# Performance work log

Hardware: AMD Instinct MI355X
Metric: run time of the kernel (lower is better)

Reference implementation:

```python
import jax, jax.numpy as jnp
import numpy as np

K = 32        # neighbors kept
SCALE = 1     # dilation stride for dilated kNN


def setup_inputs() -> dict:
    key = jax.random.key(0)
    ks = jax.random.split(key, 8)
    s = 0.05  # weight init scale
    return {
        "x": jax.random.normal(ks[0], (16, 3, 4096), jnp.float32),
        "w1": jax.random.normal(ks[1], (64, 3), jnp.float32) * s,
        "b1": jnp.zeros((64,), jnp.float32),
        "w2": jax.random.normal(ks[2], (128, 64), jnp.float32) * s,
        "b2": jnp.zeros((128,), jnp.float32),
        "w3": jax.random.normal(ks[3], (1024, 128), jnp.float32) * s,
        "b3": jnp.zeros((1024,), jnp.float32),
        "fw1": jax.random.normal(ks[4], (512, 1024), jnp.float32) * s,
        "fb1": jnp.zeros((512,), jnp.float32),
        "fw2": jax.random.normal(ks[5], (256, 512), jnp.float32) * s,
        "fb2": jnp.zeros((256,), jnp.float32),
        "fw3": jax.random.normal(ks[6], (9, 256), jnp.float32) * s,
        "fb3": jnp.zeros((9,), jnp.float32),
    }


def _knn_idx(x):
    # x: (B, C, N). Returns (B, N, K) indices of K nearest neighbors (dilated by SCALE).
    inner = jnp.einsum('bcn,bcm->bnm', x, x)            # (B, N, N)
    sq = jnp.sum(x * x, axis=1)                          # (B, N)
    neg_dist = 2.0 * inner - sq[:, :, None] - sq[:, None, :]  # = -||xi-xj||^2
    _, idx = jax.lax.top_k(neg_dist, K * SCALE)          # (B, N, K*SCALE)
    return idx[:, :, ::SCALE]                            # (B, N, K)


def reference(x, w1, b1, w2, b2, w3, b3, fw1, fb1, fw2, fb2, fw3, fb3):
    B, C, N = x.shape
    idx = _knn_idx(x)                                    # (B, N, K)
    xt = jnp.swapaxes(x, 1, 2)                           # (B, N, C)
    # gather neighbors: nbrs[b,n,k,c] = xt[b, idx[b,n,k], c]
    nbrs = jax.vmap(lambda xb, ib: xb[ib])(xt, idx)      # (B, N, K, C)
    x0 = nbrs - xt[:, :, None, :]                        # edge features x_j - x_i

    # STN (T-Net): shared MLP over edges, global max pool, FC head -> 3x3 transform
    h = jax.nn.relu(jnp.einsum('bnkc,oc->bnko', x0, w1) + b1)
    h = jax.nn.relu(jnp.einsum('bnkc,oc->bnko', h, w2) + b2)
    h = jax.nn.relu(jnp.einsum('bnkc,oc->bnko', h, w3) + b3)
    g = jnp.max(h, axis=(1, 2))                          # (B, 1024)
    f = jax.nn.relu(g @ fw1.T + fb1)
    f = jax.nn.relu(f @ fw2.T + fb2)
    t = (f @ fw3.T + fb3).reshape(B, 3, 3) + jnp.eye(3, dtype=x.dtype)

    out = jnp.einsum('bnc,bcd->bnd', xt, t)              # bmm(x^T, t)
    return jnp.swapaxes(out, 1, 2)                       # (B, 3, N)
```

## Files before the change

kernel.cpp:

```cpp
#include <hip/hip_runtime.h>
#include <hip/hip_fp8.h>

typedef __bf16 bf16_t;
typedef __bf16 bf16x8 __attribute__((ext_vector_type(8)));
typedef float floatx16 __attribute__((ext_vector_type(16)));
typedef int intx8 __attribute__((ext_vector_type(8)));
typedef unsigned long long u64;

#define B_ 16
#define N_ 4096
#define K_ 32


__device__ __forceinline__ unsigned enc_f(float f) {
    unsigned u = __float_as_uint(f);
    return (u & 0x80000000u) ? ~u : (u | 0x80000000u);
}
__device__ __forceinline__ float dec_f(unsigned e) {
    return __uint_as_float((e & 0x80000000u) ? (e & 0x7fffffffu) : ~e);
}

__global__ __launch_bounds__(512, 4) void knn_kernel(
    const float* __restrict__ x, const float* __restrict__ w3,
    const float* __restrict__ w2, unsigned short* __restrict__ idxb,
    unsigned* __restrict__ g_enc, unsigned char* __restrict__ w3f8,
    bf16_t* __restrict__ w2sw)
{
    __shared__ __align__(16) float4 cand[16 * 257];
    unsigned* lists = (unsigned*)cand;
    unsigned* m1 = ((unsigned*)cand) + 8192;
    const int tid = threadIdx.x;
    const int bid = blockIdx.x;

    {
        const int g = bid * 512 + tid;
        if (g < 131072) {
            const int q = g & 15, lI = (g >> 4) & 63, mt2 = (g >> 10) & 3, cb = g >> 12;
            const int lmI = lI & 31, hiI = lI >> 5;
            const int ch = mt2 * 32 + (q & 3) + 8 * (q >> 2) + 4 * hiI;
            __hip_fp8_e4m3 t(16.0f * w3[(cb * 32 + lmI) * 128 + ch]);
            w3f8[g] = t.__x;
        } else if (g < 139264) {
            const int o = g - 131072;
            const int f = o >> 9, r = o & 511, lI = r >> 3, jj = r & 7;
            const int ks = f & 3, nb = f >> 2, lmI = lI & 31, hiI = lI >> 5;
            w2sw[o] = (bf16_t)w2[(nb * 32 + lmI) * 64 + ks * 16 + hiI * 8 + jj];
        } else if (g < 155648) {
            g_enc[g - 139264] = 0u;
        }
    }

    const int b  = bid >> 7;
    const int q  = tid >> 4;
    const int n  = (bid & 127) * 32 + q;
    const int t  = tid & 15;
    const float* xb = x + b * 3 * N_;

    for (int j = tid; j < N_; j += 512) {
        float cx = xb[j], cy = xb[N_ + j], cz = xb[2 * N_ + j];
        cand[j + (j >> 8)] = make_float4(-2.f * cx, -2.f * cy, -2.f * cz,
                                         fmaf(cx, cx, fmaf(cy, cy, cz * cz)));
    }
    __syncthreads();

    const float xi0 = xb[n], xi1 = xb[N_ + n], xi2 = xb[2 * N_ + n];
    const float xisq1 = fmaf(xi0, xi0, fmaf(xi1, xi1, xi2 * xi2)) + 1.0f;

    unsigned r[8];
    #pragma unroll
    for (int s = 0; s < 8; s++) r[s] = 0x7F7FFFFFu;

    const int j0 = t * 256;
    const int pb = t * 257;
    #pragma unroll 8
    for (int jj = 0; jj < 256; jj++) {
        const float4 c = cand[pb + jj];
        const float d = fmaf(c.z, xi2, fmaf(c.y, xi1, fmaf(c.x, xi0, c.w)));
        const unsigned key =
            (__float_as_uint(d + xisq1) & 0xFFFFF000u) | (unsigned)(j0 + jj);
        #pragma unroll
        for (int s = 7; s >= 1; s--) {
            const unsigned hv = r[s - 1] > key ? r[s - 1] : key;
            r[s] = r[s] < hv ? r[s] : hv;
        }
        r[0] = r[0] < key ? r[0] : key;
    }
    __syncthreads();

    #pragma unroll
    for (int k = 0; k < 8; k++) lists[tid * 9 + k] = r[k];
    __syncthreads();

    if (tid < 128) {
        const int q1 = tid >> 2, gi = tid & 3;
        const int base = (q1 * 16 + gi * 4) * 9;
        unsigned h0 = lists[base], h1 = lists[base + 9];
        unsigned h2 = lists[base + 18], h3 = lists[base + 27];
        int p0 = 0, p1 = 0, p2 = 0, p3 = 0;
        unsigned* outp = m1 + (q1 * 4 + gi) * 32;
        #pragma unroll 1
        for (int k = 0; k < 32; k++) {
            const unsigned m01 = h0 < h1 ? h0 : h1;
            const unsigned m23 = h2 < h3 ? h2 : h3;
            const unsigned v = m01 < m23 ? m01 : m23;
            outp[k] = v;
            if (m01 < m23) {
                if (h1 < h0) { p1++; h1 = p1 < 8 ? lists[base + 9 + p1] : 0xFFFFFFFFu; }
                else         { p0++; h0 = p0 < 8 ? lists[base + p0]     : 0xFFFFFFFFu; }
            } else {
                if (h3 < h2) { p3++; h3 = p3 < 8 ? lists[base + 27 + p3] : 0xFFFFFFFFu; }
                else         { p2++; h2 = p2 < 8 ? lists[base + 18 + p2] : 0xFFFFFFFFu; }
            }
        }
    }
    __syncthreads();

    if (tid < 32) {
        const unsigned* g0 = m1 + tid * 128;
        unsigned h0 = g0[0], h1 = g0[32], h2 = g0[64], h3 = g0[96];
        int p0 = 0, p1 = 0, p2 = 0, p3 = 0;
        const int nq = (bid & 127) * 32 + tid;
        unsigned short* op = idxb + ((size_t)(b * N_ + nq)) * K_;
        #pragma unroll 1
        for (int k = 0; k < K_; k++) {
            const unsigned m01 = h0 < h1 ? h0 : h1;
            const unsigned m23 = h2 < h3 ? h2 : h3;
            const unsigned v = m01 < m23 ? m01 : m23;
            op[k] = (unsigned short)(v & 0xFFFu);
            if (m01 < m23) {
                if (h1 < h0) { p1++; h1 = p1 < 32 ? g0[32 + p1] : 0xFFFFFFFFu; }
                else         { p0++; h0 = p0 < 32 ? g0[p0]      : 0xFFFFFFFFu; }
            } else {
                if (h3 < h2) { p3++; h3 = p3 < 32 ? g0[96 + p3] : 0xFFFFFFFFu; }
                else         { p2++; h2 = p2 < 32 ? g0[64 + p2] : 0xFFFFFFFFu; }
            }
        }
    }
}

__device__ __forceinline__ void chunk_epilogue(
    const floatx16& a0, const floatx16& a1, int cb, unsigned* gl, int lm)
{
    float c0 = fmaxf(a0[0], a1[0]);
    float c1 = fmaxf(a0[1], a1[1]);
    float c2 = fmaxf(a0[2], a1[2]);
    float c3 = fmaxf(a0[3], a1[3]);
    #pragma unroll
    for (int o = 4; o < 16; o += 4) {
        c0 = fmaxf(fmaxf(a0[o + 0], a1[o + 0]), c0);
        c1 = fmaxf(fmaxf(a0[o + 1], a1[o + 1]), c1);
        c2 = fmaxf(fmaxf(a0[o + 2], a1[o + 2]), c2);
        c3 = fmaxf(fmaxf(a0[o + 3], a1[o + 3]), c3);
    }
    const float m = fmaxf(fmaxf(c0, c1), fmaxf(c2, c3));
    atomicMax(&gl[cb * 32 + lm], enc_f(m));
}

__global__ __launch_bounds__(256, 3) void mlp_kernel(
    const float* __restrict__ x, const unsigned short* __restrict__ idxb,
    const float* __restrict__ w1, const float* __restrict__ b1,
    const float* __restrict__ b2,
    const bf16_t* __restrict__ w2sw, const unsigned char* __restrict__ w3f8,
    unsigned* __restrict__ g_enc)
{
    __shared__ unsigned gl[1024];
    __shared__ __align__(16) float4 w1l[64];
    __shared__ __align__(16) float b2s[128];

    const int tid = threadIdx.x;
    const int b   = blockIdx.x >> 9;
    const int p0  = (blockIdx.x & 511) * 8;
    const float* xb = x + b * 3 * N_;

    const int wv = tid >> 6;
    const int l  = tid & 63;
    const int lm = l & 31;
    const int hi = l >> 5;

    for (int i = tid; i < 1024; i += 256) gl[i] = 0u;
    if (tid < 64)
        w1l[tid] = make_float4(w1[tid * 3], w1[tid * 3 + 1], w1[tid * 3 + 2], b1[tid]);
    else if (tid < 192)
        b2s[tid - 64] = 256.0f * b2[tid - 64];
    __syncthreads();

    const uint4* w3v = (const uint4*)w3f8;
    intx8 bwA[2], bwB[2];
    #pragma unroll
    for (int mt2 = 0; mt2 < 4; mt2++) {
        const uint4 v = w3v[mt2 * 64 + l];
        bwA[mt2 >> 1][(mt2 & 1) * 4 + 0] = (int)v.x;
        bwA[mt2 >> 1][(mt2 & 1) * 4 + 1] = (int)v.y;
        bwA[mt2 >> 1][(mt2 & 1) * 4 + 2] = (int)v.z;
        bwA[mt2 >> 1][(mt2 & 1) * 4 + 3] = (int)v.w;
    }

    bf16x8 b1h[2][4];
    float d0[2], d1[2], d2[2];
    #pragma unroll
    for (int nt2 = 0; nt2 < 2; nt2++) {
        const int pp = p0 + wv * 2 + nt2;
        const int j  = idxb[((size_t)(b * N_ + pp)) * K_ + lm];
        d0[nt2] = xb[j]          - xb[pp];
        d1[nt2] = xb[N_ + j]     - xb[N_ + pp];
        d2[nt2] = xb[2 * N_ + j] - xb[2 * N_ + pp];
    }
    #pragma unroll
    for (int ks = 0; ks < 4; ks++)
        #pragma unroll
        for (int jj = 0; jj < 8; jj++) {
            const float4 w = w1l[ks * 16 + hi * 8 + jj];
            #pragma unroll
            for (int nt2 = 0; nt2 < 2; nt2++)
                b1h[nt2][ks][jj] = (bf16_t)fmaxf(
                    fmaf(w.z, d2[nt2], fmaf(w.y, d1[nt2], fmaf(w.x, d0[nt2], w.w))), 0.f);
        }

    intx8 a3v[2][2];
    #pragma unroll
    for (int mt2 = 0; mt2 < 4; mt2++) {
        floatx16 acc0 = (floatx16)0.f, acc1 = (floatx16)0.f;
        #pragma unroll
        for (int ks = 0; ks < 4; ks++) {
            const bf16x8 aw = *(const bf16x8*)&w2sw[((mt2 * 4 + ks) * 64 + l) * 8];
            acc0 = __builtin_amdgcn_mfma_f32_32x32x16_bf16(aw, b1h[0][ks], acc0, 0, 0, 0);
            acc1 = __builtin_amdgcn_mfma_f32_32x32x16_bf16(aw, b1h[1][ks], acc1, 0, 0, 0);
        }
        const int kq = mt2 >> 1, c0 = (mt2 & 1) * 4;
        #pragma unroll
        for (int i2 = 0; i2 < 4; i2++) {
            const float4 bb = *(const float4*)&b2s[mt2 * 32 + i2 * 8 + hi * 4];
            {
                const float v0 = fmaxf(fmaf(acc0[4 * i2 + 0], 256.f, bb.x), 0.f);
                const float v1 = fmaxf(fmaf(acc0[4 * i2 + 1], 256.f, bb.y), 0.f);
                const float v2 = fmaxf(fmaf(acc0[4 * i2 + 2], 256.f, bb.z), 0.f);
                const float v3 = fmaxf(fmaf(acc0[4 * i2 + 3], 256.f, bb.w), 0.f);
                int w = __builtin_amdgcn_cvt_pk_fp8_f32(v0, v1, 0, false);
                w = __builtin_amdgcn_cvt_pk_fp8_f32(v2, v3, w, true);
                a3v[0][kq][c0 + i2] = w;
            }
            {
                const float v0 = fmaxf(fmaf(acc1[4 * i2 + 0], 256.f, bb.x), 0.f);
                const float v1 = fmaxf(fmaf(acc1[4 * i2 + 1], 256.f, bb.y), 0.f);
                const float v2 = fmaxf(fmaf(acc1[4 * i2 + 2], 256.f, bb.z), 0.f);
                const float v3 = fmaxf(fmaf(acc1[4 * i2 + 3], 256.f, bb.w), 0.f);
                int w = __builtin_amdgcn_cvt_pk_fp8_f32(v0, v1, 0, false);
                w = __builtin_amdgcn_cvt_pk_fp8_f32(v2, v3, w, true);
                a3v[1][kq][c0 + i2] = w;
            }
        }
    }

    const floatx16 zf = (floatx16)0.f;

#define PREFETCH_W3(dst, c) do {                                              \
        _Pragma("unroll")                                                     \
        for (int mt2 = 0; mt2 < 4; mt2++) {                                   \
            const uint4 v = w3v[((c) * 4 + mt2) * 64 + l];                    \
            dst[mt2 >> 1][(mt2 & 1) * 4 + 0] = (int)v.x;                      \
            dst[mt2 >> 1][(mt2 & 1) * 4 + 1] = (int)v.y;                      \
            dst[mt2 >> 1][(mt2 & 1) * 4 + 2] = (int)v.z;                      \
            dst[mt2 >> 1][(mt2 & 1) * 4 + 3] = (int)v.w;                      \
        } } while (0)

#define COMPUTE_W3(d0_, d1_, buf) do {                                        \
        __builtin_amdgcn_s_setprio(1);                                        \
        d0_ = __builtin_amdgcn_mfma_scale_f32_32x32x64_f8f6f4(                \
            a3v[0][0], buf[0], zf, 0, 0, 0, 0x7F7F7F7F, 0, 0x7F7F7F7F);       \
        d1_ = __builtin_amdgcn_mfma_scale_f32_32x32x64_f8f6f4(                \
            a3v[1][0], buf[0], zf, 0, 0, 0, 0x7F7F7F7F, 0, 0x7F7F7F7F);       \
        d0_ = __builtin_amdgcn_mfma_scale_f32_32x32x64_f8f6f4(                \
            a3v[0][1], buf[1], d0_, 0, 0, 0, 0x7F7F7F7F, 0, 0x7F7F7F7F);      \
        d1_ = __builtin_amdgcn_mfma_scale_f32_32x32x64_f8f6f4(                \
            a3v[1][1], buf[1], d1_, 0, 0, 0, 0x7F7F7F7F, 0, 0x7F7F7F7F);      \
        __builtin_amdgcn_s_setprio(0); } while (0)

    floatx16 pA0, pA1, pB0, pB1;

    PREFETCH_W3(bwB, 1);
    COMPUTE_W3(pA0, pA1, bwA);

    #pragma unroll 1
    for (int cc = 0; cc < 15; cc++) {
        PREFETCH_W3(bwA, 2 * cc + 2);
        COMPUTE_W3(pB0, pB1, bwB);
        chunk_epilogue(pA0, pA1, 2 * cc, gl, lm);
        PREFETCH_W3(bwB, 2 * cc + 3);
        COMPUTE_W3(pA0, pA1, bwA);
        chunk_epilogue(pB0, pB1, 2 * cc + 1, gl, lm);
    }
    COMPUTE_W3(pB0, pB1, bwB);
    chunk_epilogue(pA0, pA1, 30, gl, lm);
    chunk_epilogue(pB0, pB1, 31, gl, lm);

#undef PREFETCH_W3
#undef COMPUTE_W3

    __syncthreads();
    for (int i = tid; i < 1024; i += 256)
        atomicMax(&g_enc[b * 1024 + i], gl[i]);
}

__global__ __launch_bounds__(256) void head_kernel(
    const unsigned* __restrict__ g_enc, const float* __restrict__ b3,
    const float* __restrict__ fw1, const float* __restrict__ fb1,
    const float* __restrict__ fw2, const float* __restrict__ fb2,
    const float* __restrict__ fw3, const float* __restrict__ fb3,
    float* __restrict__ tmat)
{
    __shared__ __align__(16) float g[1024];
    __shared__ __align__(16) float f1[512];
    __shared__ __align__(16) float f2[256];
    const int t = threadIdx.x, b = blockIdx.x;

    for (int i = t; i < 1024; i += 256)
        g[i] = fmaxf(fmaf(dec_f(g_enc[b * 1024 + i]), 2.44140625e-4f, b3[i]), 0.f);
    __syncthreads();

    for (int o = t; o < 512; o += 256) {
        const float4* wr = (const float4*)(fw1 + (size_t)o * 1024);
        const float4* gv = (const float4*)g;
        float acc = fb1[o];
        for (int i = 0; i < 256; i++) {
            float4 a = wr[i], c = gv[i];
            acc = fmaf(a.x, c.x, acc); acc = fmaf(a.y, c.y, acc);
            acc = fmaf(a.z, c.z, acc); acc = fmaf(a.w, c.w, acc);
        }
        f1[o] = fmaxf(acc, 0.f);
    }
    __syncthreads();
    {
        const int o = t;
        const float4* wr = (const float4*)(fw2 + (size_t)o * 512);
        const float4* fv = (const float4*)f1;
        float acc = fb2[o];
        for (int i = 0; i < 128; i++) {
            float4 a = wr[i], c = fv[i];
            acc = fmaf(a.x, c.x, acc); acc = fmaf(a.y, c.y, acc);
            acc = fmaf(a.z, c.z, acc); acc = fmaf(a.w, c.w, acc);
        }
        f2[o] = fmaxf(acc, 0.f);
    }
    __syncthreads();
    if (t < 9) {
        const float4* wr = (const float4*)(fw3 + (size_t)t * 256);
        const float4* fv = (const float4*)f2;
        float acc = fb3[t];
        for (int i = 0; i < 64; i++) {
            float4 a = wr[i], c = fv[i];
            acc = fmaf(a.x, c.x, acc); acc = fmaf(a.y, c.y, acc);
            acc = fmaf(a.z, c.z, acc); acc = fmaf(a.w, c.w, acc);
        }
        if (t == 0 || t == 4 || t == 8) acc += 1.f;
        tmat[b * 9 + t] = acc;
    }
}

__global__ __launch_bounds__(256) void out_kernel(
    const float* __restrict__ x, const float* __restrict__ tmat,
    float* __restrict__ out)
{
    const int gid = blockIdx.x * 256 + threadIdx.x;
    const int b = gid >> 12, n = gid & 4095;
    const float* T = tmat + b * 9;
    const float x0 = x[b * 12288 + n];
    const float x1 = x[b * 12288 + 4096 + n];
    const float x2 = x[b * 12288 + 8192 + n];
    #pragma unroll
    for (int d = 0; d < 3; d++)
        out[b * 12288 + d * 4096 + n] =
            fmaf(x2, T[6 + d], fmaf(x1, T[3 + d], x0 * T[d]));
}

extern "C" void kernel_launch(void* const* d_in, const int* in_sizes, int n_in,
                              void* d_out, int out_size, void* d_ws, size_t ws_size,
                              hipStream_t stream) {
    const float* x   = (const float*)d_in[0];
    const float* w1  = (const float*)d_in[1];
    const float* b1  = (const float*)d_in[2];
    const float* w2  = (const float*)d_in[3];
    const float* b2  = (const float*)d_in[4];
    const float* w3  = (const float*)d_in[5];
    const float* b3  = (const float*)d_in[6];
    const float* fw1 = (const float*)d_in[7];
    const float* fb1 = (const float*)d_in[8];
    const float* fw2 = (const float*)d_in[9];
    const float* fb2 = (const float*)d_in[10];
    const float* fw3 = (const float*)d_in[11];
    const float* fb3 = (const float*)d_in[12];
    float* out = (float*)d_out;

    char* ws = (char*)d_ws;
    unsigned short* idxb = (unsigned short*)ws;
    unsigned* g_enc = (unsigned*)(ws + 4194304);
    unsigned char* w3f8 = (unsigned char*)(ws + 4259840);
    bf16_t* w2sw = (bf16_t*)(ws + 4390912);
    float* tmat  = (float*)(ws + 4407296);

    knn_kernel<<<2048, 512, 0, stream>>>(x, w3, w2, idxb, g_enc, w3f8, w2sw);
    mlp_kernel<<<8192, 256, 0, stream>>>(x, idxb, w1, b1, b2, w2sw, w3f8, g_enc);
    head_kernel<<<16, 256, 0, stream>>>(g_enc, b3, fw1, fb1, fw2, fb2, fw3, fb3, tmat);
    out_kernel<<<256, 256, 0, stream>>>(x, tmat, out);
}
```

Before: 560.1 us.

## Replace per-candidate insertion with batched sorting-network merge in kNN; repack fp8 w3 layout

The kNN scan now takes candidates in groups of eight. Each group is sorted with an odd-even merge network, and the running top-8 is merged with it through a bitonic min and cleanup network, replacing the per-candidate insertion chain. This cuts the serial compare dependency per candidate and drops the unroll-8 insertion loop. Separately, the fp8 w3 weights are repacked so each lane reads two contiguous 32-byte intx8 vectors instead of four uint4 loads plus element shuffles. The merge costs about the same number of compares per batch but has more parallelism; the risk is higher register pressure.

```diff
diff --git a/kernel.cpp b/kernel.cpp
--- a/kernel.cpp
+++ b/kernel.cpp
@@ -18,6 +18,12 @@
 }
 __device__ __forceinline__ float dec_f(unsigned e) {
     return __uint_as_float((e & 0x80000000u) ? (e & 0x7fffffffu) : ~e);
+}
+
+__device__ __forceinline__ void ce(unsigned& a, unsigned& b) {
+    const unsigned mn = a < b ? a : b;
+    const unsigned mx = a < b ? b : a;
+    a = mn; b = mx;
 }
 
 __global__ __launch_bounds__(512, 4) void knn_kernel(
@@ -35,7 +41,11 @@
     {
         const int g = bid * 512 + tid;
         if (g < 131072) {
-            const int q = g & 15, lI = (g >> 4) & 63, mt2 = (g >> 10) & 3, cb = g >> 12;
+            const int j  = g & 31;
+            const int lI = (g >> 5) & 63;
+            const int kq = (g >> 11) & 1;
+            const int cb = g >> 12;
+            const int mt2 = kq * 2 + (j >> 4), q = j & 15;
             const int lmI = lI & 31, hiI = lI >> 5;
             const int ch = mt2 * 32 + (q & 3) + 8 * (q >> 2) + 4 * hiI;
             __hip_fp8_e4m3 t(16.0f * w3[(cb * 32 + lmI) * 128 + ch]);
@@ -72,18 +82,31 @@
 
     const int j0 = t * 256;
     const int pb = t * 257;
-    #pragma unroll 8
-    for (int jj = 0; jj < 256; jj++) {
-        const float4 c = cand[pb + jj];
-        const float d = fmaf(c.z, xi2, fmaf(c.y, xi1, fmaf(c.x, xi0, c.w)));
-        const unsigned key =
-            (__float_as_uint(d + xisq1) & 0xFFFFF000u) | (unsigned)(j0 + jj);
-        #pragma unroll
-        for (int s = 7; s >= 1; s--) {
-            const unsigned hv = r[s - 1] > key ? r[s - 1] : key;
-            r[s] = r[s] < hv ? r[s] : hv;
-        }
-        r[0] = r[0] < key ? r[0] : key;
+    #pragma unroll 1
+    for (int jb = 0; jb < 256; jb += 8) {
+        unsigned k[8];
+        #pragma unroll
+        for (int u = 0; u < 8; u++) {
+            const float4 c = cand[pb + jb + u];
+            const float d = fmaf(c.z, xi2, fmaf(c.y, xi1, fmaf(c.x, xi0, c.w)));
+            k[u] = (__float_as_uint(d + xisq1) & 0xFFFFF000u)
+                 | (unsigned)(j0 + jb + u);
+        }
+        ce(k[0], k[1]); ce(k[2], k[3]); ce(k[4], k[5]); ce(k[6], k[7]);
+        ce(k[0], k[2]); ce(k[1], k[3]); ce(k[4], k[6]); ce(k[5], k[7]);
+        ce(k[1], k[2]); ce(k[5], k[6]);
+        ce(k[0], k[4]); ce(k[1], k[5]); ce(k[2], k[6]); ce(k[3], k[7]);
+        ce(k[2], k[4]); ce(k[3], k[5]);
+        ce(k[1], k[2]); ce(k[3], k[4]); ce(k[5], k[6]);
+        unsigned s[8];
+        #pragma unroll
+        for (int u = 0; u < 8; u++)
+            s[u] = r[u] < k[7 - u] ? r[u] : k[7 - u];
+        ce(s[0], s[4]); ce(s[1], s[5]); ce(s[2], s[6]); ce(s[3], s[7]);
+        ce(s[0], s[2]); ce(s[1], s[3]); ce(s[4], s[6]); ce(s[5], s[7]);
+        ce(s[0], s[1]); ce(s[2], s[3]); ce(s[4], s[5]); ce(s[6], s[7]);
+        #pragma unroll
+        for (int u = 0; u < 8; u++) r[u] = s[u];
     }
     __syncthreads();
 
@@ -184,16 +207,14 @@
         b2s[tid - 64] = 256.0f * b2[tid - 64];
     __syncthreads();
 
-    const uint4* w3v = (const uint4*)w3f8;
+    const unsigned char* w3p = w3f8 + l * 32;
+#define PREFETCH_W3(dst, c) do {                                              \
+        dst[0] = *(const intx8*)(w3p + (c) * 4096);                           \
+        dst[1] = *(const intx8*)(w3p + (c) * 4096 + 2048);                    \
+    } while (0)
+
     intx8 bwA[2], bwB[2];
-    #pragma unroll
-    for (int mt2 = 0; mt2 < 4; mt2++) {
-        const uint4 v = w3v[mt2 * 64 + l];
-        bwA[mt2 >> 1][(mt2 & 1) * 4 + 0] = (int)v.x;
-        bwA[mt2 >> 1][(mt2 & 1) * 4 + 1] = (int)v.y;
-        bwA[mt2 >> 1][(mt2 & 1) * 4 + 2] = (int)v.z;
-        bwA[mt2 >> 1][(mt2 & 1) * 4 + 3] = (int)v.w;
-    }
+    PREFETCH_W3(bwA, 0);
 
     bf16x8 b1h[2][4];
     float d0[2], d1[2], d2[2];
@@ -253,16 +274,6 @@
 
     const floatx16 zf = (floatx16)0.f;
 
-#define PREFETCH_W3(dst, c) do {                                              \
-        _Pragma("unroll")                                                     \
-        for (int mt2 = 0; mt2 < 4; mt2++) {                                   \
-            const uint4 v = w3v[((c) * 4 + mt2) * 64 + l];                    \
-            dst[mt2 >> 1][(mt2 & 1) * 4 + 0] = (int)v.x;                      \
-            dst[mt2 >> 1][(mt2 & 1) * 4 + 1] = (int)v.y;                      \
-            dst[mt2 >> 1][(mt2 & 1) * 4 + 2] = (int)v.z;                      \
-            dst[mt2 >> 1][(mt2 & 1) * 4 + 3] = (int)v.w;                      \
-        } } while (0)
-
 #define COMPUTE_W3(d0_, d1_, buf) do {                                        \
         __builtin_amdgcn_s_setprio(1);                                        \
         d0_ = __builtin_amdgcn_mfma_scale_f32_32x32x64_f8f6f4(                \
```

After: 522.1 us. 1.07x faster.
